# Kernel optimization log

Hardware: AMD Instinct MI355X
Metric: run time of the kernel (lower is better)

The kernel has to match this reference:

```python
import jax, jax.numpy as jnp
import numpy as np

EPS = 1e-09

def setup_inputs() -> dict:
    key = jax.random.key(0)
    k1, k2 = jax.random.split(key)
    N, C = 65536, 1024
    pred = jax.random.normal(k1, (N, C), dtype=jnp.float32)
    target = jax.random.randint(k2, (N,), 0, C, dtype=jnp.int64)
    return {"pred": pred, "target": target}

def reference(pred, target):
    # Faithful to the torch module: softmax over dim=0 (across the batch dim)
    p = jax.nn.softmax(pred, axis=0) + EPS  # epsilon added before BOTH log terms
    C = pred.shape[1]
    tar = jax.nn.one_hot(target, C, dtype=pred.dtype)  # [N, C]
    # per-row BCE with log base 2, mean over classes
    bce = tar * jnp.log2(p) + (1.0 - tar) * jnp.log2(1.0 - p)
    loss = -jnp.mean(bce, axis=1)  # [N]
    return jnp.mean(loss)
```

## Files before the change

### kernel.cpp

```cpp
#include <hip/hip_runtime.h>
#include <math.h>

static constexpr int N = 65536;
static constexpr int C = 1024;
static constexpr float EPS = 1e-9f;


template <int RPB>
__global__ __launch_bounds__(256) void colsum_partial_kernel(
    const float* __restrict__ pred, const int* __restrict__ tgt,
    float* __restrict__ partial, float* __restrict__ sxArr,
    int* __restrict__ counter) {
    const int tid  = threadIdx.x;
    const int row0 = blockIdx.x * RPB;
    if (blockIdx.x == 0 && tid == 0) *counter = 0;

    __shared__ int tgt_lds[RPB];
    if (tid < RPB) tgt_lds[tid] = tgt[row0 + tid];
    __syncthreads();

    const float4* __restrict__ p4 =
        reinterpret_cast<const float4*>(pred) + (size_t)row0 * (C / 4) + tid;

    float a0 = 0.f, a1 = 0.f, a2 = 0.f, a3 = 0.f;
    float sx = 0.f;
#pragma unroll 1
    for (int b = 0; b < RPB / 8; ++b) {
        float4 v0 = p4[0 * (C / 4)];
        float4 v1 = p4[1 * (C / 4)];
        float4 v2 = p4[2 * (C / 4)];
        float4 v3 = p4[3 * (C / 4)];
        float4 v4 = p4[4 * (C / 4)];
        float4 v5 = p4[5 * (C / 4)];
        float4 v6 = p4[6 * (C / 4)];
        float4 v7 = p4[7 * (C / 4)];
        p4 += 8 * (C / 4);
        __builtin_amdgcn_sched_barrier(0);

#pragma unroll
        for (int r = 0; r < 8; ++r) {
            const int tc = tgt_lds[b * 8 + r];
            if ((tc >> 2) == tid) {
                const float4 v = (r == 0) ? v0 : (r == 1) ? v1 : (r == 2) ? v2
                               : (r == 3) ? v3 : (r == 4) ? v4 : (r == 5) ? v5
                               : (r == 6) ? v6 : v7;
                const int sel = tc & 3;
                sx += (sel == 0) ? v.x : (sel == 1) ? v.y : (sel == 2) ? v.z : v.w;
            }
        }

        a0 += __expf(v0.x) + __expf(v1.x) + __expf(v2.x) + __expf(v3.x)
            + __expf(v4.x) + __expf(v5.x) + __expf(v6.x) + __expf(v7.x);
        a1 += __expf(v0.y) + __expf(v1.y) + __expf(v2.y) + __expf(v3.y)
            + __expf(v4.y) + __expf(v5.y) + __expf(v6.y) + __expf(v7.y);
        a2 += __expf(v0.z) + __expf(v1.z) + __expf(v2.z) + __expf(v3.z)
            + __expf(v4.z) + __expf(v5.z) + __expf(v6.z) + __expf(v7.z);
        a3 += __expf(v0.w) + __expf(v1.w) + __expf(v2.w) + __expf(v3.w)
            + __expf(v4.w) + __expf(v5.w) + __expf(v6.w) + __expf(v7.w);
    }

    reinterpret_cast<float4*>(partial + (size_t)blockIdx.x * C)[tid] =
        make_float4(a0, a1, a2, a3);

#pragma unroll
    for (int off = 32; off > 0; off >>= 1)
        sx += __shfl_down(sx, off, 64);
    __shared__ float wsum[4];
    if ((tid & 63) == 0) wsum[tid >> 6] = sx;
    __syncthreads();
    if (tid == 0)
        sxArr[blockIdx.x] = wsum[0] + wsum[1] + wsum[2] + wsum[3];
}

__global__ __launch_bounds__(256) void reduce_gather_kernel(
    const float* __restrict__ partial, const int* __restrict__ tgt,
    const float* __restrict__ sxArr, float* __restrict__ logS,
    int* __restrict__ counter, float* __restrict__ out, int RB) {
    const int t  = threadIdx.x;
    const int cp = t & 7;
    const int r0 = t >> 3;
    const int c0 = blockIdx.x * 16;
    const int eighth = RB / 8;

    const float2* __restrict__ p2 =
        reinterpret_cast<const float2*>(partial) + (c0 >> 1) + cp;

    float2 a[8];
#pragma unroll
    for (int j = 0; j < 8; ++j) a[j] = make_float2(0.f, 0.f);
    for (int r = r0; r < eighth; r += 32) {
#pragma unroll
        for (int j = 0; j < 8; ++j) {
            const float2 v = p2[(size_t)(r + j * eighth) * (C / 2)];
            a[j].x += v.x;
            a[j].y += v.y;
        }
    }
    float2 s;
    s.x = ((a[0].x + a[1].x) + (a[2].x + a[3].x)) + ((a[4].x + a[5].x) + (a[6].x + a[7].x));
    s.y = ((a[0].y + a[1].y) + (a[2].y + a[3].y)) + ((a[4].y + a[5].y) + (a[6].y + a[7].y));
#pragma unroll
    for (int off = 8; off <= 32; off <<= 1) {
        s.x += __shfl_xor(s.x, off, 64);
        s.y += __shfl_xor(s.y, off, 64);
    }
    __shared__ float2 wred[4][8];
    if ((t & 63) < 8) wred[t >> 6][cp] = s;
    __syncthreads();
    if (t < 8) {
        const float vx = wred[0][t].x + wred[1][t].x + wred[2][t].x + wred[3][t].x;
        const float vy = wred[0][t].y + wred[1][t].y + wred[2][t].y + wred[3][t].y;
        __hip_atomic_store(&logS[c0 + 2 * t],     log2f(vx),
                           __ATOMIC_RELEASE, __HIP_MEMORY_SCOPE_AGENT);
        __hip_atomic_store(&logS[c0 + 2 * t + 1], log2f(vy),
                           __ATOMIC_RELEASE, __HIP_MEMORY_SCOPE_AGENT);
        __threadfence();
    }
    __syncthreads();

    __shared__ int last;
    if (t == 0) {
        const int old = __hip_atomic_fetch_add(counter, 1, __ATOMIC_ACQ_REL,
                                               __HIP_MEMORY_SCOPE_AGENT);
        last = (old == (int)gridDim.x - 1) ? 1 : 0;
    }
    __syncthreads();
    if (!last) return;

    __shared__ float lut[C];
    for (int i = t; i < C; i += 256)
        lut[i] = __hip_atomic_load(&logS[i], __ATOMIC_RELAXED,
                                   __HIP_MEMORY_SCOPE_AGENT);
    __syncthreads();

    float accL = 0.f;
    for (int n = t; n < N; n += 256 * 8) {
        accL += lut[tgt[n + 256 * 0]] + lut[tgt[n + 256 * 1]]
              + lut[tgt[n + 256 * 2]] + lut[tgt[n + 256 * 3]]
              + lut[tgt[n + 256 * 4]] + lut[tgt[n + 256 * 5]]
              + lut[tgt[n + 256 * 6]] + lut[tgt[n + 256 * 7]];
    }
    float sx = 0.f;
    for (int i = t; i < RB; i += 256) sx += sxArr[i];

#pragma unroll
    for (int off = 32; off > 0; off >>= 1) {
        accL += __shfl_down(accL, off, 64);
        sx   += __shfl_down(sx, off, 64);
    }
    __shared__ float r1[4], r2[4];
    if ((t & 63) == 0) { r1[t >> 6] = accL; r2[t >> 6] = sx; }
    __syncthreads();
    if (t == 0) {
        const double LOG2E = 1.4426950408889634;
        const double SumLogS = (double)(r1[0] + r1[1] + r1[2] + r1[3]);
        const double SumX    = (double)(r2[0] + r2[1] + r2[2] + r2[3]);
        const double termA   = -LOG2E * (double)C * (1.0 + (double)N * (double)EPS);
        const double total   = termA + LOG2E * SumX - SumLogS;
        out[0] = (float)(-total / ((double)N * (double)C));
    }
}

extern "C" void kernel_launch(void* const* d_in, const int* in_sizes, int n_in,
                              void* d_out, int out_size, void* d_ws, size_t ws_size,
                              hipStream_t stream) {
    const float* pred = (const float*)d_in[0];
    const int*   tgt  = (const int*)d_in[1];
    float* wsf     = (float*)d_ws;
    float* logS    = wsf;
    int*   counter = (int*)(wsf + 1024);
    float* sxArr   = wsf + 1088;
    float* partial = wsf + 4096;
    const size_t base_bytes = 4096 * sizeof(float);

    int RB = 2048;
    while (RB > 512 && base_bytes + (size_t)RB * C * sizeof(float) > ws_size)
        RB >>= 1;

    if (RB >= 2048)
        colsum_partial_kernel<32><<<2048, 256, 0, stream>>>(pred, tgt, partial, sxArr, counter);
    else if (RB == 1024)
        colsum_partial_kernel<64><<<1024, 256, 0, stream>>>(pred, tgt, partial, sxArr, counter);
    else
        colsum_partial_kernel<128><<<512, 256, 0, stream>>>(pred, tgt, partial, sxArr, counter);

    reduce_gather_kernel<<<64, 256, 0, stream>>>(partial, tgt, sxArr, logS,
                                                 counter, (float*)d_out, RB);
}
```

Before: 71.77 us.

## Split column reduce and target gather into separate kernels with parallel gather

Result: faster. 65.03 us (-9.4%).

```diff
diff --git a/kernel.cpp b/kernel.cpp
--- a/kernel.cpp
+++ b/kernel.cpp
@@ -72,10 +72,8 @@
         sxArr[blockIdx.x] = wsum[0] + wsum[1] + wsum[2] + wsum[3];
 }
 
-__global__ __launch_bounds__(256) void reduce_gather_kernel(
-    const float* __restrict__ partial, const int* __restrict__ tgt,
-    const float* __restrict__ sxArr, float* __restrict__ logS,
-    int* __restrict__ counter, float* __restrict__ out, int RB) {
+__global__ __launch_bounds__(256) void colreduce_kernel(
+    const float* __restrict__ partial, float* __restrict__ logS, int RB) {
     const int t  = threadIdx.x;
     const int cp = t & 7;
     const int r0 = t >> 3;
@@ -110,16 +108,28 @@
     if (t < 8) {
         const float vx = wred[0][t].x + wred[1][t].x + wred[2][t].x + wred[3][t].x;
         const float vy = wred[0][t].y + wred[1][t].y + wred[2][t].y + wred[3][t].y;
-        __hip_atomic_store(&logS[c0 + 2 * t],     log2f(vx),
-                           __ATOMIC_RELEASE, __HIP_MEMORY_SCOPE_AGENT);
-        __hip_atomic_store(&logS[c0 + 2 * t + 1], log2f(vy),
-                           __ATOMIC_RELEASE, __HIP_MEMORY_SCOPE_AGENT);
-        __threadfence();
+        logS[c0 + 2 * t]     = log2f(vx);
+        logS[c0 + 2 * t + 1] = log2f(vy);
     }
+}
+
+__global__ __launch_bounds__(256) void gather_finalize_kernel(
+    const int* __restrict__ tgt, const float* __restrict__ logS,
+    const float* __restrict__ sxArr, float* __restrict__ gArr,
+    int* __restrict__ counter, float* __restrict__ out, int RB) {
+    const int t = threadIdx.x;
+    float v = logS[tgt[blockIdx.x * 256 + t]];
+#pragma unroll
+    for (int off = 32; off > 0; off >>= 1)
+        v += __shfl_down(v, off, 64);
+    __shared__ float wsum[4];
+    if ((t & 63) == 0) wsum[t >> 6] = v;
     __syncthreads();
 
     __shared__ int last;
     if (t == 0) {
+        gArr[blockIdx.x] = wsum[0] + wsum[1] + wsum[2] + wsum[3];
+        __threadfence();
         const int old = __hip_atomic_fetch_add(counter, 1, __ATOMIC_ACQ_REL,
                                                __HIP_MEMORY_SCOPE_AGENT);
         last = (old == (int)gridDim.x - 1) ? 1 : 0;
@@ -127,29 +137,17 @@
     __syncthreads();
     if (!last) return;
 
-    __shared__ float lut[C];
-    for (int i = t; i < C; i += 256)
-        lut[i] = __hip_atomic_load(&logS[i], __ATOMIC_RELAXED,
-                                   __HIP_MEMORY_SCOPE_AGENT);
-    __syncthreads();
-
-    float accL = 0.f;
-    for (int n = t; n < N; n += 256 * 8) {
-        accL += lut[tgt[n + 256 * 0]] + lut[tgt[n + 256 * 1]]
-              + lut[tgt[n + 256 * 2]] + lut[tgt[n + 256 * 3]]
-              + lut[tgt[n + 256 * 4]] + lut[tgt[n + 256 * 5]]
-              + lut[tgt[n + 256 * 6]] + lut[tgt[n + 256 * 7]];
-    }
+    float gl = __hip_atomic_load(&gArr[t], __ATOMIC_RELAXED,
+                                 __HIP_MEMORY_SCOPE_AGENT);
     float sx = 0.f;
     for (int i = t; i < RB; i += 256) sx += sxArr[i];
-
 #pragma unroll
     for (int off = 32; off > 0; off >>= 1) {
-        accL += __shfl_down(accL, off, 64);
-        sx   += __shfl_down(sx, off, 64);
+        gl += __shfl_down(gl, off, 64);
+        sx += __shfl_down(sx, off, 64);
     }
     __shared__ float r1[4], r2[4];
-    if ((t & 63) == 0) { r1[t >> 6] = accL; r2[t >> 6] = sx; }
+    if ((t & 63) == 0) { r1[t >> 6] = gl; r2[t >> 6] = sx; }
     __syncthreads();
     if (t == 0) {
         const double LOG2E = 1.4426950408889634;
@@ -170,6 +168,7 @@
     float* logS    = wsf;
     int*   counter = (int*)(wsf + 1024);
     float* sxArr   = wsf + 1088;
+    float* gArr    = wsf + 3200;
     float* partial = wsf + 4096;
     const size_t base_bytes = 4096 * sizeof(float);
 
@@ -184,6 +183,7 @@
     else
         colsum_partial_kernel<128><<<512, 256, 0, stream>>>(pred, tgt, partial, sxArr, counter);
 
-    reduce_gather_kernel<<<64, 256, 0, stream>>>(partial, tgt, sxArr, logS,
-                                                 counter, (float*)d_out, RB);
+    colreduce_kernel<<<64, 256, 0, stream>>>(partial, logS, RB);
+    gather_finalize_kernel<<<256, 256, 0, stream>>>(tgt, logS, sxArr, gArr,
+                                                    counter, (float*)d_out, RB);
 }
```
